# Performance work log

Hardware: AMD Instinct MI355X
Metric: run time of the kernel (lower is better)

Reference implementation:

```python
import jax, jax.numpy as jnp
import numpy as np

B, T, D, H, E = 2, 1024, 1024, 4096, 8


def setup_inputs() -> dict:
    key = jax.random.key(0)
    ks = jax.random.split(key, 7)
    s = 0.02  # weight init scale
    return {
        "x": jax.random.normal(ks[0], (B, T, D), jnp.float32),
        "gate_w": jax.random.normal(ks[1], (D, E), jnp.float32) * s,
        "gate_b": jnp.zeros((E,), jnp.float32),
        "w1": jax.random.normal(ks[2], (E, D, H), jnp.float32) * s,
        "b1": jnp.zeros((E, H), jnp.float32),
        "w2": jax.random.normal(ks[3], (E, H, D), jnp.float32) * s,
        "b2": jnp.zeros((E, D), jnp.float32),
    }


def reference(x, gate_w, gate_b, w1, b1, w2, b2):
    b, t, d = x.shape
    e = gate_w.shape[1]
    xt = x.reshape(b * t, d)                      # [N, D]
    logits = xt @ gate_w + gate_b                 # [N, E]
    probs = jax.nn.softmax(logits, axis=-1)
    top_expert = jnp.argmax(probs, axis=-1)       # [N]
    onehot = jax.nn.one_hot(top_expert, e, dtype=x.dtype)  # [N, E]
    # dense per-expert FFN, then combine via top-1 one-hot (same math as masked dispatch)
    h = jax.nn.gelu(jnp.einsum('nd,edh->enh', xt, w1) + b1[:, None, :], approximate=False)  # [E, N, H]
    y = jnp.einsum('enh,ehd->end', h, w2) + b2[:, None, :]                                  # [E, N, D]
    out = jnp.einsum('end,ne->nd', y, onehot).reshape(b, t, d)
    counts = jnp.sum(onehot, axis=0)              # [E], float
    frac = counts / jnp.maximum(counts.sum(), 1.0)
    aux_loss = jnp.mean((frac - 1.0 / e) ** 2)
    return out, aux_loss
```

## Files before the change

kernel.cpp:

```cpp
#include <hip/hip_runtime.h>
#include <stdint.h>

#define N_TOK 2048
#define DDIM 1024
#define HDIM 4096
#define NEXP 8
#define BM 128
#define MAXT 24
#define PADCAP 3072

#define C_COUNTS 0
#define C_CURSOR 8
#define C_PADOFF 16
#define C_TILECNT 25
#define C_TILE_E 32
#define C_TILE_M0 56
#define C_TILE_ROWS 80
#define C_EXPERT 128
#define C_PERM 2176

#define XG_OFF 32768
#define HG_OFF (XG_OFF + PADCAP*DDIM*2)

typedef float f32x4 __attribute__((ext_vector_type(4)));
typedef short s16x8 __attribute__((ext_vector_type(8)));
typedef unsigned int u32;
typedef unsigned short u16;

__device__ __forceinline__ u16 f2bf(float f){
  u32 u = __float_as_uint(f);
  u += 0x7fffu + ((u >> 16) & 1u);
  return (u16)(u >> 16);
}

__device__ __forceinline__ u32 pkbf(float a, float b){
  u32 r; asm("v_cvt_pk_bf16_f32 %0, %1, %2" : "=v"(r) : "v"(a), "v"(b)); return r;
}

__device__ __forceinline__ void gl_lds16(const void* g, void* l){
  __builtin_amdgcn_global_load_lds((const __attribute__((address_space(1))) u32*)g,
                                   (__attribute__((address_space(3))) u32*)l, 16, 0, 0);
}

__global__ __launch_bounds__(256) void gate_kern(
    const float* __restrict__ x, const float* __restrict__ gw,
    const float* __restrict__ gb, int* __restrict__ ctrl)
{
  const int wv = threadIdx.x >> 6, l = threadIdx.x & 63;
  const int n = blockIdx.x * 4 + wv;
  const float* xr = x + (size_t)n * DDIM;
  float acc[NEXP];
  #pragma unroll
  for (int e = 0; e < NEXP; e++) acc[e] = 0.f;
  #pragma unroll 4
  for (int i = 0; i < DDIM/64; i++){
    int k = i*64 + l;
    float xv = xr[k];
    const float* g = gw + (size_t)k * NEXP;
    #pragma unroll
    for (int e = 0; e < NEXP; e++) acc[e] = fmaf(xv, g[e], acc[e]);
  }
  #pragma unroll
  for (int e = 0; e < NEXP; e++){
    #pragma unroll
    for (int off = 32; off > 0; off >>= 1) acc[e] += __shfl_xor(acc[e], off);
  }
  if (l == 0){
    float best = acc[0] + gb[0]; int bi = 0;
    #pragma unroll
    for (int e = 1; e < NEXP; e++){
      float v = acc[e] + gb[e];
      if (v > best){ best = v; bi = e; }
    }
    ctrl[C_EXPERT + n] = bi;
    atomicAdd(&ctrl[C_COUNTS + bi], 1);
  }
}

__global__ void setup_kern(int* __restrict__ ctrl, float* __restrict__ aux_out)
{
  const int t = threadIdx.x;
  for (int i = t; i < PADCAP; i += 256) ctrl[C_PERM + i] = -1;
  if (t == 0){
    int off = 0, tc = 0;
    float aux = 0.f;
    for (int e = 0; e < NEXP; e++){
      int c = ctrl[C_COUNTS + e];
      ctrl[C_PADOFF + e] = off;
      ctrl[C_CURSOR + e] = off;
      int nt = (c + BM - 1) / BM;
      for (int j = 0; j < nt; j++){
        ctrl[C_TILE_E   + tc] = e;
        ctrl[C_TILE_M0  + tc] = off + j*BM;
        ctrl[C_TILE_ROWS+ tc] = min(BM, c - j*BM);
        tc++;
      }
      off += nt * BM;
      float fr = (float)c * (1.f/(float)N_TOK);
      float d = fr - 1.f/(float)NEXP;
      aux += d*d;
    }
    ctrl[C_TILECNT] = tc;
    *aux_out = aux * (1.f/(float)NEXP);
  }
}

__global__ __launch_bounds__(256) void scatter_kern(int* __restrict__ ctrl)
{
  const int n = blockIdx.x * 256 + threadIdx.x;
  const int e = ctrl[C_EXPERT + n];
  const int pos = atomicAdd(&ctrl[C_CURSOR + e], 1);
  ctrl[C_PERM + pos] = n;
}

__global__ __launch_bounds__(256) void xg_kern(
    const float* __restrict__ x, const int* __restrict__ ctrl,
    u16* __restrict__ Xg)
{
  const int slot = blockIdx.x, t = threadIdx.x;
  const int tok = ctrl[C_PERM + slot];
  ushort4 o;
  if (tok >= 0){
    f32x4 v = *(const f32x4*)(x + (size_t)tok*DDIM + t*4);
    o.x = f2bf(v.x); o.y = f2bf(v.y); o.z = f2bf(v.z); o.w = f2bf(v.w);
  } else { o.x = 0; o.y = 0; o.z = 0; o.w = 0; }
  *(ushort4*)(Xg + (size_t)slot*DDIM + t*4) = o;
}

template<int MODE>
__global__ __launch_bounds__(256, 4) void moe_gemm(
    const u16* __restrict__ Ag, const float* __restrict__ W,
    const float* __restrict__ bias, u16* __restrict__ Hg,
    float* __restrict__ outp, const int* __restrict__ ctrl)
{
  constexpr int K    = (MODE==1) ? DDIM : HDIM;
  constexpr int NN   = (MODE==1) ? HDIM : DDIM;
  constexpr int KS   = (MODE==1) ? 1 : 4;
  constexpr int KLOC = K / KS;
  constexpr int BN   = 64;
  constexpr int BK   = 32;
  constexpr int NF   = BN / 32;
  constexpr int CPR  = BK / 8;
  constexpr int AVM  = (BM*BK)/(256*8);
  constexpr int BCPR = BN / 4;
  constexpr int BVM  = (BK*BN)/(256*4);
  constexpr int NT   = KLOC / BK;

  const int by = blockIdx.y;
  if (by >= ctrl[C_TILECNT]) return;
  const int e    = ctrl[C_TILE_E + by];
  const int m0   = ctrl[C_TILE_M0 + by];
  const int rows = ctrl[C_TILE_ROWS + by];
  const int n0   = blockIdx.x * BN;
  const int kb   = (MODE==1) ? 0 : blockIdx.z * KLOC;

  const int tid = threadIdx.x;
  const int w = tid >> 6, l = tid & 63;
  const int wr = w >> 1, wc = w & 1;
  const int lhi = l >> 4, llo = l & 15;

  __shared__ __align__(16) u16   As[2][BM*BK];
  __shared__ __align__(16) float Bs[2][BK*BN];
  __shared__ int perm_s[BM];

  if constexpr (MODE == 2){
    if (tid < BM) perm_s[tid] = ctrl[C_PERM + m0 + tid];
  }

  f32x4 acc[4][NF];
  #pragma unroll
  for (int mf = 0; mf < 4; mf++)
    #pragma unroll
    for (int nf = 0; nf < NF; nf++) acc[mf][nf] = (f32x4){0.f,0.f,0.f,0.f};

  const u16* Abase = Ag + (size_t)m0 * K;
  int arow[AVM], apos[AVM];
  #pragma unroll
  for (int i = 0; i < AVM; i++){
    int f = i*256 + tid;
    arow[i] = f / CPR;
    apos[i] = (f & (CPR-1)) ^ (arow[i] & (CPR-1));
  }
  const float* Wb = W + (size_t)e * K * NN + n0;
  int brow[BVM], bpos[BVM];
  #pragma unroll
  for (int i = 0; i < BVM; i++){
    int f = i*256 + tid;
    brow[i] = f / BCPR;
    bpos[i] = (f % BCPR) ^ (((brow[i] >> 3) & 1) << 2);
  }

  const int col0 = wc*(BN/2) + llo;
  const int bswz = (lhi & 1) << 2;

#define STAGE_A(buf, k0) { \
    u16* ad = &As[buf][(w*64)*8]; \
    _Pragma("unroll") \
    for (int i = 0; i < AVM; i++) \
      gl_lds16(Abase + (size_t)arow[i]*K + (k0) + apos[i]*8, ad + i*256*8); }

#define STAGE_B(buf, k0) { \
    float* bd = &Bs[buf][(w*64)*4]; \
    _Pragma("unroll") \
    for (int i = 0; i < BVM; i++) \
      gl_lds16(Wb + (size_t)((k0) + brow[i])*NN + bpos[i]*4, bd + i*256*4); }

#define COMPUTE(buf) { \
    s16x8 a[4]; \
    _Pragma("unroll") \
    for (int mf = 0; mf < 4; mf++){ \
      int row = wr*64 + mf*16 + llo; \
      int pos = lhi ^ (row & (CPR-1)); \
      a[mf] = *(const s16x8*)&As[buf][row*BK + pos*8]; } \
    _Pragma("unroll") \
    for (int nf = 0; nf < NF; nf++){ \
      const int col = col0 + nf*16; \
      const float* bp_ = &Bs[buf][(lhi*8)*BN + \
                                  ((((col) >> 2) ^ bswz) << 2) + ((col) & 3)]; \
      union { u32 u[4]; s16x8 v; } bb_; \
      bb_.u[0] = pkbf(bp_[0*BN], bp_[1*BN]); \
      bb_.u[1] = pkbf(bp_[2*BN], bp_[3*BN]); \
      bb_.u[2] = pkbf(bp_[4*BN], bp_[5*BN]); \
      bb_.u[3] = pkbf(bp_[6*BN], bp_[7*BN]); \
      _Pragma("unroll") \
      for (int mf = 0; mf < 4; mf++) \
        acc[mf][nf] = __builtin_amdgcn_mfma_f32_16x16x32_bf16(a[mf], bb_.v, acc[mf][nf], 0, 0, 0); \
    } }

  STAGE_A(0, kb);
  STAGE_B(0, kb);
  __syncthreads();

  int cur = 0;
  #pragma unroll 1
  for (int t = 0; t < NT; t++){
    if (t+1 < NT){
      STAGE_A(cur^1, kb + (t+1)*BK);
      STAGE_B(cur^1, kb + (t+1)*BK);
    }
    COMPUTE(cur);
    __syncthreads();
    cur ^= 1;
  }

  if constexpr (MODE == 1){
    const float* bp = bias + (size_t)e*NN + n0;
    #pragma unroll
    for (int nf = 0; nf < NF; nf++){
      const int cl = wc*(BN/2) + nf*16 + llo;
      const float bb = bp[cl];
      #pragma unroll
      for (int mf = 0; mf < 4; mf++){
        #pragma unroll
        for (int r = 0; r < 4; r++){
          const int rl = wr*64 + mf*16 + lhi*4 + r;
          float vv = acc[mf][nf][r] + bb;
          float gel = 0.5f * vv * (1.0f + erff(vv * 0.70710678118f));
          Hg[(size_t)(m0+rl)*NN + n0 + cl] = f2bf(gel);
        }
      }
    }
  } else {
    const float* bp = bias + (size_t)e*NN + n0;
    const bool addb = (blockIdx.z == 0);
    #pragma unroll
    for (int mf = 0; mf < 4; mf++){
      #pragma unroll
      for (int r = 0; r < 4; r++){
        const int rl = wr*64 + mf*16 + lhi*4 + r;
        if (rl < rows){
          const int tok = perm_s[rl];
          #pragma unroll
          for (int nf = 0; nf < NF; nf++){
            const int cl = wc*(BN/2) + nf*16 + llo;
            float v = acc[mf][nf][r] + (addb ? bp[cl] : 0.f);
            atomicAdd(&outp[(size_t)tok*DDIM + n0 + cl], v);
          }
        }
      }
    }
  }
#undef STAGE_A
#undef STAGE_B
#undef COMPUTE
}

extern "C" void kernel_launch(void* const* d_in, const int* in_sizes, int n_in,
                              void* d_out, int out_size, void* d_ws, size_t ws_size,
                              hipStream_t stream)
{
  (void)in_sizes; (void)n_in; (void)out_size; (void)ws_size;
  const float* x  = (const float*)d_in[0];
  const float* gw = (const float*)d_in[1];
  const float* gb = (const float*)d_in[2];
  const float* w1 = (const float*)d_in[3];
  const float* b1 = (const float*)d_in[4];
  const float* w2 = (const float*)d_in[5];
  const float* b2 = (const float*)d_in[6];
  float* out = (float*)d_out;
  char* ws = (char*)d_ws;
  int* ctrl = (int*)ws;
  u16* Xg = (u16*)(ws + XG_OFF);
  u16* Hg = (u16*)(ws + HG_OFF);

  hipMemsetAsync(ctrl, 0, 64, stream);
  hipMemsetAsync(out, 0, (size_t)N_TOK*DDIM*4, stream);
  gate_kern<<<N_TOK/4, 256, 0, stream>>>(x, gw, gb, ctrl);
  setup_kern<<<1, 256, 0, stream>>>(ctrl, out + (size_t)N_TOK*DDIM);
  scatter_kern<<<N_TOK/256, 256, 0, stream>>>(ctrl);
  xg_kern<<<PADCAP, 256, 0, stream>>>(x, ctrl, Xg);
  moe_gemm<1><<<dim3(HDIM/64, MAXT),    256, 0, stream>>>(Xg, w1, b1, Hg, nullptr, ctrl);
  moe_gemm<2><<<dim3(DDIM/64, MAXT, 4), 256, 0, stream>>>(Hg, w2, b2, nullptr, out, ctrl);
}
```

Measured before the change: 238.4 us.

## Split MoE GEMM into producer/consumer warps with 128x128 tiles and unpadded expert layout

The MoE GEMM kernel now runs 512 threads: four producer waves stage A and B tiles into LDS while four consumer waves run the MFMA compute, and the output tile grows from 128x64 to 128x128. Expert row blocks are packed contiguously rather than padded to multiples of 128, which shrinks the gathered activation buffer and the xg launch. The goal is to overlap loads with compute and reuse each staged tile across a wider N range. The cost is that half the waves never issue MFMAs, the larger tiles halve the number of blocks, and unpadded tiles can read rows that belong to the next expert (their writes are masked by the rows check).

```diff
diff --git a/kernel.cpp b/kernel.cpp
--- a/kernel.cpp
+++ b/kernel.cpp
@@ -5,22 +5,21 @@
 #define DDIM 1024
 #define HDIM 4096
 #define NEXP 8
-#define BM 128
 #define MAXT 24
-#define PADCAP 3072
 
 #define C_COUNTS 0
 #define C_CURSOR 8
 #define C_PADOFF 16
-#define C_TILECNT 25
+#define C_TILECNT 24
 #define C_TILE_E 32
-#define C_TILE_M0 56
-#define C_TILE_ROWS 80
-#define C_EXPERT 128
-#define C_PERM 2176
-
-#define XG_OFF 32768
-#define HG_OFF (XG_OFF + PADCAP*DDIM*2)
+#define C_TILE_M0 80
+#define C_TILE_ROWS 128
+#define C_EXPERT 192
+#define C_PERM 2304
+
+#define ACAPB 2304
+#define XGB_OFF 32768
+#define HGB_OFF (XGB_OFF + ACAPB*DDIM*2)
 
 typedef float f32x4 __attribute__((ext_vector_type(4)));
 typedef short s16x8 __attribute__((ext_vector_type(8)));
@@ -80,7 +79,7 @@
 __global__ void setup_kern(int* __restrict__ ctrl, float* __restrict__ aux_out)
 {
   const int t = threadIdx.x;
-  for (int i = t; i < PADCAP; i += 256) ctrl[C_PERM + i] = -1;
+  for (int i = t; i < 2560; i += 256) ctrl[C_PERM + i] = -1;
   if (t == 0){
     int off = 0, tc = 0;
     float aux = 0.f;
@@ -88,14 +87,14 @@
       int c = ctrl[C_COUNTS + e];
       ctrl[C_PADOFF + e] = off;
       ctrl[C_CURSOR + e] = off;
-      int nt = (c + BM - 1) / BM;
+      int nt = (c + 127) / 128;
       for (int j = 0; j < nt; j++){
         ctrl[C_TILE_E   + tc] = e;
-        ctrl[C_TILE_M0  + tc] = off + j*BM;
-        ctrl[C_TILE_ROWS+ tc] = min(BM, c - j*BM);
+        ctrl[C_TILE_M0  + tc] = off + j*128;
+        ctrl[C_TILE_ROWS+ tc] = min(128, c - j*128);
         tc++;
       }
-      off += nt * BM;
+      off += c;
       float fr = (float)c * (1.f/(float)N_TOK);
       float d = fr - 1.f/(float)NEXP;
       aux += d*d;
@@ -128,7 +127,7 @@
 }
 
 template<int MODE>
-__global__ __launch_bounds__(256, 4) void moe_gemm(
+__global__ __launch_bounds__(512, 4) void moe_gemm_pc(
     const u16* __restrict__ Ag, const float* __restrict__ W,
     const float* __restrict__ bias, u16* __restrict__ Hg,
     float* __restrict__ outp, const int* __restrict__ ctrl)
@@ -137,13 +136,9 @@
   constexpr int NN   = (MODE==1) ? HDIM : DDIM;
   constexpr int KS   = (MODE==1) ? 1 : 4;
   constexpr int KLOC = K / KS;
-  constexpr int BN   = 64;
+  constexpr int BM   = 128;
+  constexpr int BN   = 128;
   constexpr int BK   = 32;
-  constexpr int NF   = BN / 32;
-  constexpr int CPR  = BK / 8;
-  constexpr int AVM  = (BM*BK)/(256*8);
-  constexpr int BCPR = BN / 4;
-  constexpr int BVM  = (BK*BN)/(256*4);
   constexpr int NT   = KLOC / BK;
 
   const int by = blockIdx.y;
@@ -156,7 +151,7 @@
 
   const int tid = threadIdx.x;
   const int w = tid >> 6, l = tid & 63;
-  const int wr = w >> 1, wc = w & 1;
+  const bool prod = (w < 4);
   const int lhi = l >> 4, llo = l & 15;
 
   __shared__ __align__(16) u16   As[2][BM*BK];
@@ -167,42 +162,41 @@
     if (tid < BM) perm_s[tid] = ctrl[C_PERM + m0 + tid];
   }
 
-  f32x4 acc[4][NF];
+  const u16*   Abase = Ag + (size_t)m0 * K;
+  const float* Wb    = W + (size_t)e * K * NN + n0;
+  int arow[2], apos[2], brow[4], bpos[4];
+  #pragma unroll
+  for (int i = 0; i < 2; i++){
+    int f = i*256 + tid;
+    arow[i] = f >> 2;
+    apos[i] = (f & 3) ^ (arow[i] & 3);
+  }
+  #pragma unroll
+  for (int i = 0; i < 4; i++){
+    int f = i*256 + tid;
+    brow[i] = f >> 5;
+    bpos[i] = (f & 31) ^ (((brow[i] >> 3) & 1) << 2);
+  }
+
+  const int cw = w - 4;
+  const int wr = cw >> 1, wc = cw & 1;
+  const int col0 = wc*64 + llo;
+  const int bswz = (lhi & 1) << 2;
+
+  f32x4 acc[4][4];
   #pragma unroll
   for (int mf = 0; mf < 4; mf++)
     #pragma unroll
-    for (int nf = 0; nf < NF; nf++) acc[mf][nf] = (f32x4){0.f,0.f,0.f,0.f};
-
-  const u16* Abase = Ag + (size_t)m0 * K;
-  int arow[AVM], apos[AVM];
-  #pragma unroll
-  for (int i = 0; i < AVM; i++){
-    int f = i*256 + tid;
-    arow[i] = f / CPR;
-    apos[i] = (f & (CPR-1)) ^ (arow[i] & (CPR-1));
-  }
-  const float* Wb = W + (size_t)e * K * NN + n0;
-  int brow[BVM], bpos[BVM];
-  #pragma unroll
-  for (int i = 0; i < BVM; i++){
-    int f = i*256 + tid;
-    brow[i] = f / BCPR;
-    bpos[i] = (f % BCPR) ^ (((brow[i] >> 3) & 1) << 2);
-  }
-
-  const int col0 = wc*(BN/2) + llo;
-  const int bswz = (lhi & 1) << 2;
-
-#define STAGE_A(buf, k0) { \
-    u16* ad = &As[buf][(w*64)*8]; \
-    _Pragma("unroll") \
-    for (int i = 0; i < AVM; i++) \
-      gl_lds16(Abase + (size_t)arow[i]*K + (k0) + apos[i]*8, ad + i*256*8); }
-
-#define STAGE_B(buf, k0) { \
+    for (int nf = 0; nf < 4; nf++) acc[mf][nf] = (f32x4){0.f,0.f,0.f,0.f};
+
+#define STAGE(buf, k0) { \
+    u16*   ad = &As[buf][(w*64)*8]; \
     float* bd = &Bs[buf][(w*64)*4]; \
     _Pragma("unroll") \
-    for (int i = 0; i < BVM; i++) \
+    for (int i = 0; i < 2; i++) \
+      gl_lds16(Abase + (size_t)arow[i]*K + (k0) + apos[i]*8, ad + i*256*8); \
+    _Pragma("unroll") \
+    for (int i = 0; i < 4; i++) \
       gl_lds16(Wb + (size_t)((k0) + brow[i])*NN + bpos[i]*4, bd + i*256*4); }
 
 #define COMPUTE(buf) { \
@@ -210,10 +204,10 @@
     _Pragma("unroll") \
     for (int mf = 0; mf < 4; mf++){ \
       int row = wr*64 + mf*16 + llo; \
-      int pos = lhi ^ (row & (CPR-1)); \
+      int pos = lhi ^ (row & 3); \
       a[mf] = *(const s16x8*)&As[buf][row*BK + pos*8]; } \
     _Pragma("unroll") \
-    for (int nf = 0; nf < NF; nf++){ \
+    for (int nf = 0; nf < 4; nf++){ \
       const int col = col0 + nf*16; \
       const float* bp_ = &Bs[buf][(lhi*8)*BN + \
                                   ((((col) >> 2) ^ bswz) << 2) + ((col) & 3)]; \
@@ -227,61 +221,61 @@
         acc[mf][nf] = __builtin_amdgcn_mfma_f32_16x16x32_bf16(a[mf], bb_.v, acc[mf][nf], 0, 0, 0); \
     } }
 
-  STAGE_A(0, kb);
-  STAGE_B(0, kb);
+  if (prod){ STAGE(0, kb); }
   __syncthreads();
 
-  int cur = 0;
   #pragma unroll 1
   for (int t = 0; t < NT; t++){
-    if (t+1 < NT){
-      STAGE_A(cur^1, kb + (t+1)*BK);
-      STAGE_B(cur^1, kb + (t+1)*BK);
+    if (prod){
+      if (t+1 < NT){ STAGE((t+1)&1, kb + (t+1)*BK); }
+    } else {
+      COMPUTE(t&1);
     }
-    COMPUTE(cur);
     __syncthreads();
-    cur ^= 1;
-  }
-
-  if constexpr (MODE == 1){
-    const float* bp = bias + (size_t)e*NN + n0;
-    #pragma unroll
-    for (int nf = 0; nf < NF; nf++){
-      const int cl = wc*(BN/2) + nf*16 + llo;
-      const float bb = bp[cl];
+  }
+
+  if (!prod){
+    if constexpr (MODE == 1){
+      const float* bp = bias + (size_t)e*NN + n0;
+      #pragma unroll
+      for (int nf = 0; nf < 4; nf++){
+        const int cl = wc*64 + nf*16 + llo;
+        const float bb = bp[cl];
+        #pragma unroll
+        for (int mf = 0; mf < 4; mf++){
+          #pragma unroll
+          for (int r = 0; r < 4; r++){
+            const int rl = wr*64 + mf*16 + lhi*4 + r;
+            if (rl < rows){
+              float vv = acc[mf][nf][r] + bb;
+              float gel = 0.5f * vv * (1.0f + erff(vv * 0.70710678118f));
+              Hg[(size_t)(m0+rl)*NN + n0 + cl] = f2bf(gel);
+            }
+          }
+        }
+      }
+    } else {
+      const float* bp = bias + (size_t)e*NN + n0;
+      const bool addb = (blockIdx.z == 0);
       #pragma unroll
       for (int mf = 0; mf < 4; mf++){
         #pragma unroll
         for (int r = 0; r < 4; r++){
           const int rl = wr*64 + mf*16 + lhi*4 + r;
-          float vv = acc[mf][nf][r] + bb;
-          float gel = 0.5f * vv * (1.0f + erff(vv * 0.70710678118f));
-          Hg[(size_t)(m0+rl)*NN + n0 + cl] = f2bf(gel);
-        }
-      }
-    }
-  } else {
-    const float* bp = bias + (size_t)e*NN + n0;
-    const bool addb = (blockIdx.z == 0);
-    #pragma unroll
-    for (int mf = 0; mf < 4; mf++){
-      #pragma unroll
-      for (int r = 0; r < 4; r++){
-        const int rl = wr*64 + mf*16 + lhi*4 + r;
-        if (rl < rows){
-          const int tok = perm_s[rl];
-          #pragma unroll
-          for (int nf = 0; nf < NF; nf++){
-            const int cl = wc*(BN/2) + nf*16 + llo;
-            float v = acc[mf][nf][r] + (addb ? bp[cl] : 0.f);
-            atomicAdd(&outp[(size_t)tok*DDIM + n0 + cl], v);
+          if (rl < rows){
+            const int tok = perm_s[rl];
+            #pragma unroll
+            for (int nf = 0; nf < 4; nf++){
+              const int cl = wc*64 + nf*16 + llo;
+              float v = acc[mf][nf][r] + (addb ? bp[cl] : 0.f);
+              atomicAdd(&outp[(size_t)tok*DDIM + n0 + cl], v);
+            }
           }
         }
       }
     }
   }
-#undef STAGE_A
-#undef STAGE_B
+#undef STAGE
 #undef COMPUTE
 }
 
@@ -300,15 +294,16 @@
   float* out = (float*)d_out;
   char* ws = (char*)d_ws;
   int* ctrl = (int*)ws;
-  u16* Xg = (u16*)(ws + XG_OFF);
-  u16* Hg = (u16*)(ws + HG_OFF);
+  u16* Xg = (u16*)(ws + XGB_OFF);
+  u16* Hg = (u16*)(ws + HGB_OFF);
 
   hipMemsetAsync(ctrl, 0, 64, stream);
   hipMemsetAsync(out, 0, (size_t)N_TOK*DDIM*4, stream);
   gate_kern<<<N_TOK/4, 256, 0, stream>>>(x, gw, gb, ctrl);
   setup_kern<<<1, 256, 0, stream>>>(ctrl, out + (size_t)N_TOK*DDIM);
   scatter_kern<<<N_TOK/256, 256, 0, stream>>>(ctrl);
-  xg_kern<<<PADCAP, 256, 0, stream>>>(x, ctrl, Xg);
-  moe_gemm<1><<<dim3(HDIM/64, MAXT),    256, 0, stream>>>(Xg, w1, b1, Hg, nullptr, ctrl);
-  moe_gemm<2><<<dim3(DDIM/64, MAXT, 4), 256, 0, stream>>>(Hg, w2, b2, nullptr, out, ctrl);
-}
+  xg_kern<<<ACAPB, 256, 0, stream>>>(x, ctrl, Xg);
+
+  moe_gemm_pc<1><<<dim3(HDIM/128, MAXT),    512, 0, stream>>>(Xg, w1, b1, Hg, nullptr, ctrl);
+  moe_gemm_pc<2><<<dim3(DDIM/128, MAXT, 4), 512, 0, stream>>>(Hg, w2, b2, nullptr, out, ctrl);
+}
```

Measured after the change: 268.9 us. 1.13x slower.
